# Optimization experiments

Measured on AMD Instinct MI355X. Metric: run time of the kernel, lower is better.

## Reference

```python
import jax, jax.numpy as jnp
import numpy as np

H_FULL, W_FULL = 256, 704
IMG_H, IMG_W = 16, 44  # height//16, width//16
D_BINS, D_STR, D_END = 50, 1.0, 45.0
N_CAMS = 6
BEV_C = 192
VOX_STR = np.array([-40.0, -40.0, -1.0], np.float32)
VOX_END = np.array([40.0, 40.0, 5.4], np.float32)


def _frustum():
    # Faithful to create_pixel_grid: x/y built width-major, flattened, then flat-reshaped
    # to (img_h, img_w) in forward (this scrambling is intentional / matches torch .reshape).
    x = jnp.broadcast_to(jnp.linspace(0.0, W_FULL - 1.0, IMG_W)[:, None], (IMG_W, IMG_H))
    y = jnp.broadcast_to(jnp.linspace(0.0, H_FULL - 1.0, IMG_H)[None, :], (IMG_W, IMG_H))
    pix = jnp.stack([x, y], 0).reshape(2, IMG_H, IMG_W)
    pix = jnp.broadcast_to(pix[:, None], (2, D_BINS, IMG_H, IMG_W))
    d = jnp.broadcast_to(jnp.linspace(D_STR, D_END, D_BINS)[None, :, None, None], (1, D_BINS, IMG_H, IMG_W))
    return jnp.transpose(jnp.concatenate([pix, d], 0), (1, 2, 3, 0))  # [D, h, w, 3]


def trilinear_sample(vol, grid):
    # vol [B,C,D,H,W]; grid [B,Do,Ho,Wo,3] normalized (x,y,z); align_corners=True, zeros padding
    B, C, D, H, W = vol.shape
    Do, Ho, Wo = grid.shape[1:4]
    g = grid.reshape(B, -1, 3)
    P = g.shape[1]
    x = (g[..., 0] + 1.0) * 0.5 * (W - 1)
    y = (g[..., 1] + 1.0) * 0.5 * (H - 1)
    z = (g[..., 2] + 1.0) * 0.5 * (D - 1)
    x0f, y0f, z0f = jnp.floor(x), jnp.floor(y), jnp.floor(z)
    fx, fy, fz = x - x0f, y - y0f, z - z0f
    x0, y0, z0 = x0f.astype(jnp.int32), y0f.astype(jnp.int32), z0f.astype(jnp.int32)
    vol_flat = vol.reshape(B, C, D * H * W)
    gather = jax.vmap(lambda vf, i: jnp.take(vf, i, axis=1))
    out = jnp.zeros((B, C, P), vol.dtype)
    for dz in (0, 1):
        wz = fz if dz else 1.0 - fz
        iz = z0 + dz
        for dy in (0, 1):
            wy = fy if dy else 1.0 - fy
            iy = y0 + dy
            for dx in (0, 1):
                wx = fx if dx else 1.0 - fx
                ix = x0 + dx
                valid = (ix >= 0) & (ix < W) & (iy >= 0) & (iy < H) & (iz >= 0) & (iz < D)
                idx = (jnp.clip(iz, 0, D - 1) * H + jnp.clip(iy, 0, H - 1)) * W + jnp.clip(ix, 0, W - 1)
                v = gather(vol_flat, idx)  # [B,C,P]
                out = out + v * (wx * wy * wz * valid)[:, None, :]
    return out.reshape(B, C, Do, Ho, Wo)


def conv3x3(x, w, b):
    y = jax.lax.conv_general_dilated(x, w, window_strides=(1, 1), padding='SAME',
                                     dimension_numbers=('NCHW', 'OIHW', 'NCHW'))
    return y + b[None, :, None, None]


def setup_inputs() -> dict:
    key = jax.random.key(0)
    ks = jax.random.split(key, 10)
    B = 2
    eye3 = jnp.eye(3, dtype=jnp.float32)
    eye4 = jnp.eye(4, dtype=jnp.float32)
    bev_feat = jax.random.normal(ks[0], (B, BEV_C, 100, 100, 8), jnp.float32)
    imgs = jax.random.normal(ks[1], (B, N_CAMS, 3, H_FULL, W_FULL), jnp.float32)
    sensor2egos = eye4 + 0.1 * jax.random.normal(ks[2], (B, N_CAMS, 4, 4), jnp.float32)
    ego2globals = eye4 + 0.1 * jax.random.normal(ks[3], (B, N_CAMS, 4, 4), jnp.float32)
    K = jnp.array([[700.0, 0.0, 352.0], [0.0, 700.0, 128.0], [0.0, 0.0, 1.0]], jnp.float32)
    intrins = K + 1.0 * jax.random.normal(ks[4], (B, N_CAMS, 3, 3), jnp.float32)
    post_rots = eye3 + 0.01 * jax.random.normal(ks[5], (B, N_CAMS, 3, 3), jnp.float32)
    post_trans = 0.1 * jax.random.normal(ks[6], (B, N_CAMS, 3), jnp.float32)
    bda = eye3 + 0.01 * jax.random.normal(ks[7], (B, 3, 3), jnp.float32)
    enc = BEV_C * D_BINS  # 9600
    conv1_w = 0.003 * jax.random.normal(ks[8], (256, enc, 3, 3), jnp.float32)
    conv1_b = jnp.zeros((256,), jnp.float32)
    conv2_w = 0.02 * jax.random.normal(ks[9], (88, 256, 3, 3), jnp.float32)
    conv2_b = jnp.zeros((88,), jnp.float32)
    return dict(bev_feat=bev_feat, imgs=imgs, sensor2egos=sensor2egos, ego2globals=ego2globals,
                intrins=intrins, post_rots=post_rots, post_trans=post_trans, bda=bda,
                conv1_w=conv1_w, conv1_b=conv1_b, conv2_w=conv2_w, conv2_b=conv2_b)


def reference(bev_feat, imgs, sensor2egos, ego2globals, intrins, post_rots, post_trans, bda,
              conv1_w, conv1_b, conv2_w, conv2_b):
    B = imgs.shape[0]
    vol = jnp.transpose(bev_feat, (0, 1, 4, 3, 2))  # [B,C,Z,Y,X] -> grid_sample (x=W, y=H, z=D)
    fr = _frustum()[None, None]  # [1,1,D,h,w,3]
    pts = fr - post_trans[:, :, None, None, None, :]  # [B,6,D,h,w,3]
    pts = jnp.einsum('bnij,bndhwj->bndhwi', jnp.linalg.inv(post_rots), pts)
    pts = jnp.concatenate([pts[..., :2] * pts[..., 2:3], pts[..., 2:3]], -1)
    pts = jnp.einsum('bnij,bndhwj->bndhwi', jnp.linalg.inv(intrins[:, :N_CAMS]), pts)
    N = D_BINS * IMG_H * IMG_W
    cam = pts.reshape(B, N_CAMS, 3, N)  # faithful flat reshape (same semantics as torch .reshape)
    cam = jnp.concatenate([cam, jnp.ones((B, N_CAMS, 1, N), cam.dtype)], 2)
    ego = jnp.einsum('bnij,bnjp->bnip', sensor2egos[:, :N_CAMS, :3, :], cam)
    ego = jnp.einsum('bij,bnjp->bnip', bda, ego)
    g = jnp.transpose(ego, (0, 1, 3, 2))  # [B,6,N,3]
    vs = jnp.asarray(VOX_STR)
    vl = jnp.asarray(VOX_END - VOX_STR)
    g = (g - vs) / vl * 2.0 - 1.0
    g = g.reshape(B, N_CAMS * D_BINS, IMG_H, IMG_W, 3)  # batch all cams into the depth axis
    s = trilinear_sample(vol, g)  # [B,C,6*D,h,w]
    s = s.reshape(B, BEV_C, N_CAMS, D_BINS, IMG_H, IMG_W)
    s = jnp.transpose(s, (0, 2, 1, 3, 4, 5)).reshape(B * N_CAMS, BEV_C * D_BINS, IMG_H, IMG_W)
    x = jax.nn.relu(conv3x3(s, conv1_w, conv1_b))
    x = jax.nn.relu(conv3x3(x, conv2_w, conv2_b))
    return x  # [B*6, 88, 16, 44] == stack(dim=1).flatten(0,1)
```

## Files before the change

kernel.cpp:

```cpp
#include <hip/hip_runtime.h>
#include <hip/hip_bf16.h>
#include <hip/hip_fp16.h>
#include <stdint.h>

typedef __attribute__((ext_vector_type(8))) short s16x8;
typedef __attribute__((ext_vector_type(4))) float f32x4;
#define BF16 __hip_bfloat16

#define VM0 asm volatile("s_waitcnt vmcnt(0)" ::: "memory")

__device__ __forceinline__ void gload16(void* lds, const void* g) {
  __builtin_amdgcn_global_load_lds((const __attribute__((address_space(1))) void*)g,
                                   (__attribute__((address_space(3))) void*)lds, 16, 0, 0);
}

__device__ __forceinline__ short f2bf(float f) {
  union { __hip_bfloat16 h; short s; } u; u.h = __float2bfloat16(f); return u.s;
}

__device__ __forceinline__ void inv3(const float* m, float* o) {
  float a00=m[0],a01=m[1],a02=m[2],a10=m[3],a11=m[4],a12=m[5],a20=m[6],a21=m[7],a22=m[8];
  float c00 = a11*a22 - a12*a21;
  float c01 = a12*a20 - a10*a22;
  float c02 = a10*a21 - a11*a20;
  float det = a00*c00 + a01*c01 + a02*c02;
  float id = 1.0f/det;
  o[0]=c00*id; o[1]=(a02*a21-a01*a22)*id; o[2]=(a01*a12-a02*a11)*id;
  o[3]=c01*id; o[4]=(a00*a22-a02*a20)*id; o[5]=(a02*a10-a00*a12)*id;
  o[6]=c02*id; o[7]=(a01*a20-a00*a21)*id; o[8]=(a00*a11-a01*a10)*id;
}

__global__ __launch_bounds__(192) void k_prep_vol(const float* __restrict__ bev, BF16* __restrict__ volT) {
  int blk = blockIdx.x;
  int b = blk / 10000, xy = blk % 10000;
  int t = threadIdx.x;
  __shared__ alignas(16) BF16 sm[1536];
  const float* src = bev + (((size_t)b*192 + t)*10000 + xy)*8;
#pragma unroll
  for (int z = 0; z < 8; ++z) sm[z*192 + t] = __float2bfloat16(src[z]);
  __syncthreads();
  BF16* dst = volT + (size_t)blk*1536;
  *reinterpret_cast<s16x8*>(&dst[t*8]) = *reinterpret_cast<const s16x8*>(&sm[t*8]);
}

__global__ __launch_bounds__(256) void k_prep_w1(const float* __restrict__ w1, BF16* __restrict__ A1) {
  int blk = blockIdx.x;
  int oc = blk / 6, c0 = (blk % 6) * 32;
  __shared__ short sm[18000];
  int t = threadIdx.x;
  const float* src = w1 + (size_t)oc*86400 + (size_t)c0*450;
  for (int i = 0; i < 15; ++i) {
    int f4 = i*256 + t;
    if (f4 < 3600) {
      float4 v = *((const float4*)src + f4);
      int flat = f4*4;
#pragma unroll
      for (int q = 0; q < 4; ++q) {
        int fl = flat + q;
        int c = fl / 450, r = fl % 450, dd = r / 9, sg = r % 9;
        float vq = (q==0)?v.x:(q==1)?v.y:(q==2)?v.z:v.w;
        sm[(sg*50 + dd)*40 + c] = f2bf(vq);
      }
    }
  }
  __syncthreads();
  BF16* dstbase = A1 + (size_t)oc*86400 + c0;
  for (int i = 0; i < 8; ++i) {
    int fw = i*256 + t;
    if (fw < 1800) {
      int sdd = fw >> 2, q4 = fw & 3;
      int sg = sdd / 50, dd = sdd % 50;
      s16x8 v = *(const s16x8*)&sm[sdd*40 + q4*8];
      *(s16x8*)&dstbase[(size_t)sg*9600 + dd*192 + q4*8] = v;
    }
  }
}

__global__ __launch_bounds__(256) void k_prep_w2(const float* __restrict__ w2, BF16* __restrict__ w2T) {
  unsigned o = blockIdx.x*256u + threadIdx.x;
  unsigned oc = o / 2304u; unsigned r = o % 2304u;
  unsigned seg = r / 256u; unsigned c = r % 256u;
  float v = (oc < 88u) ? w2[(oc*256u + c)*9u + seg] : 0.0f;
  w2T[o] = __float2bfloat16(v);
}

__global__ __launch_bounds__(256) void k_geom(const float* __restrict__ s2e, const float* __restrict__ intr,
                       const float* __restrict__ prots, const float* __restrict__ ptrans,
                       const float* __restrict__ bda, float* __restrict__ geom) {
  int tid = blockIdx.x*256 + threadIdx.x;
  int p = tid % 35200; int bn = tid / 35200;
  int b = bn / 6;
  float PR[9], IN[9], iPR[9], iIN[9], BD[9], SE[12], PT[3];
#pragma unroll
  for (int i = 0; i < 9; ++i) { PR[i] = prots[bn*9+i]; IN[i] = intr[bn*9+i]; BD[i] = bda[b*9+i]; }
#pragma unroll
  for (int i = 0; i < 12; ++i) SE[i] = s2e[bn*16+i];
#pragma unroll
  for (int i = 0; i < 3; ++i) PT[i] = ptrans[bn*3+i];
  inv3(PR, iPR); inv3(IN, iIN);
  float cam[3];
#pragma unroll
  for (int c3 = 0; c3 < 3; ++c3) {
    int f = c3*35200 + p;
    int comp = f % 3; int t1 = f / 3;
    int w = t1 % 44;  int t2 = t1 / 44;
    int h = t2 % 16;  int dd = t2 / 16;
    int hw = h*44 + w;
    float px = 703.0f*(float)(hw >> 4)*(1.0f/43.0f);
    float py = 17.0f*(float)(hw & 15);
    float dv = 1.0f + 44.0f*(float)dd*(1.0f/49.0f);
    float t0 = px - PT[0], t1f = py - PT[1], t2f = dv - PT[2];
    float ux = iPR[0]*t0 + iPR[1]*t1f + iPR[2]*t2f;
    float uy = iPR[3]*t0 + iPR[4]*t1f + iPR[5]*t2f;
    float uz = iPR[6]*t0 + iPR[7]*t1f + iPR[8]*t2f;
    float m0 = ux*uz, m1 = uy*uz, m2 = uz;
    cam[c3] = iIN[comp*3+0]*m0 + iIN[comp*3+1]*m1 + iIN[comp*3+2]*m2;
  }
  float e0 = SE[0]*cam[0] + SE[1]*cam[1] + SE[2]*cam[2] + SE[3];
  float e1 = SE[4]*cam[0] + SE[5]*cam[1] + SE[6]*cam[2] + SE[7];
  float e2 = SE[8]*cam[0] + SE[9]*cam[1] + SE[10]*cam[2] + SE[11];
  float q0 = BD[0]*e0 + BD[1]*e1 + BD[2]*e2;
  float q1 = BD[3]*e0 + BD[4]*e1 + BD[5]*e2;
  float q2 = BD[6]*e0 + BD[7]*e1 + BD[8]*e2;
  float gx = (q0 + 40.0f)*(1.0f/80.0f)*2.0f - 1.0f;
  float gy = (q1 + 40.0f)*(1.0f/80.0f)*2.0f - 1.0f;
  float gz = (q2 + 1.0f)*(1.0f/6.4f)*2.0f - 1.0f;
  float* o = geom + (size_t)tid*3;
  o[0] = (gx + 1.0f)*0.5f*99.0f;
  o[1] = (gy + 1.0f)*0.5f*99.0f;
  o[2] = (gz + 1.0f)*0.5f*7.0f;
}

__global__ __launch_bounds__(256) void k_sample(const BF16* __restrict__ volT, const float* __restrict__ geom,
                         BF16* __restrict__ s_p) {
  unsigned tid = blockIdx.x*256u + threadIdx.x;
  unsigned cg8 = (tid % 24u) * 8u;
  unsigned q   = tid / 24u;
  unsigned dd  = q % 50u;  unsigned q2 = q / 50u;
  unsigned pix = q2 % 704u; unsigned bn = q2 / 704u;
  unsigned b = bn / 6u;
  const float* g = geom + ((size_t)bn*35200 + dd*704 + pix)*3;
  float X = g[0], Y = g[1], Z = g[2];
  float xf = floorf(X), yf = floorf(Y), zf = floorf(Z);
  int x0 = (int)xf, y0 = (int)yf, z0 = (int)zf;
  float fx = X - xf, fy = Y - yf, fz = Z - zf;
  float acc[8] = {0,0,0,0,0,0,0,0};
#pragma unroll
  for (int dz = 0; dz < 2; ++dz) {
    int iz = z0 + dz; float wz = dz ? fz : 1.0f - fz;
    bool vz = (iz >= 0) && (iz < 8);
    int cz = min(max(iz, 0), 7);
#pragma unroll
    for (int dy = 0; dy < 2; ++dy) {
      int iy = y0 + dy; float wy = dy ? fy : 1.0f - fy;
      bool vy = vz && (iy >= 0) && (iy < 100);
      int cy = min(max(iy, 0), 99);
#pragma unroll
      for (int dx = 0; dx < 2; ++dx) {
        int ix = x0 + dx; float wx = dx ? fx : 1.0f - fx;
        bool vv = vy && (ix >= 0) && (ix < 100);
        int cx = min(max(ix, 0), 99);
        float wgt = wx*wy*wz;
        if (vv && wgt != 0.0f) {
          s16x8 v = *(const s16x8*)&volT[((((size_t)b*100 + cx)*100 + cy)*8 + cz)*192 + cg8];
#pragma unroll
          for (int j = 0; j < 8; ++j) {
            unsigned u = (unsigned)(unsigned short)v[j];
            acc[j] += wgt * __uint_as_float(u << 16);
          }
        }
      }
    }
  }
  s16x8 o;
#pragma unroll
  for (int j = 0; j < 8; ++j) o[j] = f2bf(acc[j]);
  *(s16x8*)&s_p[((size_t)bn*704 + pix)*9600 + dd*192 + cg8] = o;
}

#define G1_NS 180
__global__ __launch_bounds__(256) void k_gemm1(const BF16* __restrict__ A1, const BF16* __restrict__ s_p,
                        const BF16* __restrict__ zpage, __half* __restrict__ part) {
  int gid = blockIdx.x;
  int ks = gid % 15; int t0 = gid / 15;
  int nt = t0 % 6;   t0 /= 6;
  int mt = t0 & 1;   int bn = t0 >> 1;
  int oc0 = mt*128, pix0 = nt*128;
  int tid = threadIdx.x, wv = tid >> 6, lane = tid & 63;
  int wr = wv >> 1, wc = wv & 1;
  __shared__ alignas(16) short lA0s[4096], lA1s[4096], lB0s[4096], lB1s[4096];
  int lr15 = lane & 15, kq8 = (lane >> 4)*8;
  int k0 = ks*5760;
  const BF16* gA0 = A1 + (size_t)(oc0 + wv*32 + lr15)*86400 + k0 + kq8;
  const BF16* gA1 = gA0 + (size_t)16*86400;
  int prow0 = pix0 + wv*32 + lr15;
  int prow1 = prow0 + 16;
  int ph0p = prow0/44, pw0p = prow0%44;
  int ph1p = prow1/44, pw1p = prow1%44;
  int seg  = k0 / 9600;
  int kloc = k0 - seg*9600;
  const BF16 *gB0, *gB1; int inc0, inc1;
  {
    int dh = seg/3 - 1, dw = seg%3 - 1;
    { int qh = ph0p+dh, qw = pw0p+dw;
      bool v = (prow0<704)&&(qh>=0)&&(qh<16)&&(qw>=0)&&(qw<44);
      gB0 = v ? s_p + ((size_t)bn*704 + qh*44+qw)*9600 + kloc + kq8 : zpage + kq8; inc0 = v?32:0; }
    { int qh = ph1p+dh, qw = pw1p+dw;
      bool v = (prow1<704)&&(qh>=0)&&(qh<16)&&(qw>=0)&&(qw<44);
      gB1 = v ? s_p + ((size_t)bn*704 + qh*44+qw)*9600 + kloc + kq8 : zpage + kq8; inc1 = v?32:0; }
  }
#define G1_STAGE(LA, LB) { gload16(&LA[wv*1024], gA0); gload16(&LA[wv*1024+512], gA1); \
                           gload16(&LB[wv*1024], gB0); gload16(&LB[wv*1024+512], gB1); }
#define G1_BUMP() { gA0 += 32; gA1 += 32; gB0 += inc0; gB1 += inc1; kloc += 32; \
    if (kloc == 9600) { kloc = 0; seg++; int sg = seg < 9 ? seg : 8; \
      int dh = sg/3 - 1, dw = sg%3 - 1; \
      { int qh = ph0p+dh, qw = pw0p+dw; bool v = (prow0<704)&&(qh>=0)&&(qh<16)&&(qw>=0)&&(qw<44); \
        gB0 = v ? s_p + ((size_t)bn*704 + qh*44+qw)*9600 + kq8 : zpage + kq8; inc0 = v?32:0; } \
      { int qh = ph1p+dh, qw = pw1p+dw; bool v = (prow1<704)&&(qh>=0)&&(qh<16)&&(qw>=0)&&(qw<44); \
        gB1 = v ? s_p + ((size_t)bn*704 + qh*44+qw)*9600 + kq8 : zpage + kq8; inc1 = v?32:0; } } }
  f32x4 acc[4][4] = {};
  int ra = wr*2048 + lane*8;
  int rb = wc*2048 + lane*8;
#define G1_COMPUTE(LA, LB) { s16x8 af[4], bfv[4]; \
    _Pragma("unroll") for (int m = 0; m < 4; ++m) af[m]  = *(const s16x8*)&LA[ra + m*512]; \
    _Pragma("unroll") for (int n = 0; n < 4; ++n) bfv[n] = *(const s16x8*)&LB[rb + n*512]; \
    _Pragma("unroll") for (int m = 0; m < 4; ++m) \
    _Pragma("unroll") for (int n = 0; n < 4; ++n) \
      acc[m][n] = __builtin_amdgcn_mfma_f32_16x16x32_bf16(af[m], bfv[n], acc[m][n], 0, 0, 0); }

  G1_STAGE(lA0s, lB0s); G1_BUMP();
  VM0;
  __syncthreads();
  for (int t = 0; t < G1_NS; t += 2) {
    G1_STAGE(lA1s, lB1s); G1_BUMP();
    G1_COMPUTE(lA0s, lB0s);
    VM0;
    __syncthreads();
    if (t + 2 < G1_NS) { G1_STAGE(lA0s, lB0s); G1_BUMP(); }
    G1_COMPUTE(lA1s, lB1s);
    VM0;
    __syncthreads();
  }
#pragma unroll
  for (int m = 0; m < 4; ++m) {
    int ocb = oc0 + wr*64 + m*16 + ((lane >> 4) << 2);
#pragma unroll
    for (int n = 0; n < 4; ++n) {
      int px = pix0 + wc*64 + n*16 + lr15;
      if (px < 704) {
        __half* dst = part + (((size_t)ks*12 + bn)*256 + ocb)*704 + px;
#pragma unroll
        for (int r = 0; r < 4; ++r) dst[(size_t)r*704] = __float2half(acc[m][n][r]);
      }
    }
  }
}

__global__ __launch_bounds__(256) void k_reduce1(const __half* __restrict__ part, const float* __restrict__ b1,
                          BF16* __restrict__ out1p) {
  int bn = blockIdx.x / 44; int pg = blockIdx.x % 44; int pix0 = pg*16;
  int t = threadIdx.x;
  __shared__ float sm[4096];
  for (int f = t; f < 4096; f += 256) {
    int oc = f >> 4, pl = f & 15;
    float s = 0.0f;
#pragma unroll
    for (int ks = 0; ks < 15; ++ks)
      s += __half2float(part[(((size_t)ks*12 + bn)*256 + oc)*704 + pix0 + pl]);
    s += b1[oc];
    sm[f] = fmaxf(s, 0.0f);
  }
  __syncthreads();
  for (int f = t; f < 4096; f += 256) {
    int pl = f >> 8;
    int oc = f & 255;
    out1p[((size_t)bn*704 + pix0 + pl)*256 + oc] = __float2bfloat16(sm[oc*16 + pl]);
  }
}

__global__ __launch_bounds__(256) void k_gemm2(const BF16* __restrict__ w2T, const BF16* __restrict__ x1,
                        const BF16* __restrict__ zpage, const float* __restrict__ b2,
                        float* __restrict__ out) {
  int gid = blockIdx.x;
  int nt = gid % 11, bn = gid / 11;
  int pix0 = nt*64;
  int tid = threadIdx.x, wv = tid >> 6, lane = tid & 63;
  int wr = wv >> 1, wc = wv & 1;
  __shared__ alignas(16) short lA[3072];
  __shared__ alignas(16) short lB[2048];
  int lr15 = lane & 15, kq8 = (lane >> 4)*8;
  const BF16* gA0 = w2T + (size_t)(wv*16 + lr15)*2304 + kq8;
  const BF16* gA1 = w2T + (size_t)((4+wv)*16 + lr15)*2304 + kq8;
  int prow = pix0 + wv*16 + lr15;
  int ph0 = prow/44, pw0 = prow%44;
  f32x4 acc[3][2] = {};
  for (int seg = 0; seg < 9; ++seg) {
    int dh = seg/3 - 1, dw = seg%3 - 1;
    int qh = ph0 + dh, qw = pw0 + dw;
    bool v = (qh >= 0) && (qh < 16) && (qw >= 0) && (qw < 44);
    const BF16* gB = v ? x1 + ((size_t)bn*704 + qh*44 + qw)*256 + kq8 : zpage + kq8;
    int incB = v ? 32 : 0;
    for (int s = 0; s < 8; ++s) {
      __syncthreads();
      gload16(&lA[wv*512], gA0);
      if (wv < 2) gload16(&lA[(4+wv)*512], gA1);
      gload16(&lB[wv*512], gB);
      VM0;
      __syncthreads();
      s16x8 af[3], bfv[2];
#pragma unroll
      for (int m = 0; m < 3; ++m) af[m]  = *(const s16x8*)&lA[(wr*3+m)*512 + lane*8];
#pragma unroll
      for (int n = 0; n < 2; ++n) bfv[n] = *(const s16x8*)&lB[(wc*2+n)*512 + lane*8];
#pragma unroll
      for (int m = 0; m < 3; ++m)
#pragma unroll
        for (int n = 0; n < 2; ++n)
          acc[m][n] = __builtin_amdgcn_mfma_f32_16x16x32_bf16(af[m], bfv[n], acc[m][n], 0, 0, 0);
      gA0 += 32; gA1 += 32; gB += incB;
    }
  }
#pragma unroll
  for (int m = 0; m < 3; ++m) {
    int ocb = wr*48 + m*16 + ((lane >> 4) << 2);
#pragma unroll
    for (int n = 0; n < 2; ++n) {
      int px = pix0 + wc*32 + n*16 + lr15;
#pragma unroll
      for (int r = 0; r < 4; ++r) {
        int oc = ocb + r;
        if (oc < 88)
          out[((size_t)bn*88 + oc)*704 + px] = fmaxf(acc[m][n][r] + b2[oc], 0.0f);
      }
    }
  }
}

extern "C" void kernel_launch(void* const* d_in, const int* in_sizes, int n_in,
                              void* d_out, int out_size, void* d_ws, size_t ws_size,
                              hipStream_t stream) {
  (void)in_sizes; (void)n_in; (void)out_size;
  const float* bev   = (const float*)d_in[0];
  const float* s2e   = (const float*)d_in[2];
  const float* intr  = (const float*)d_in[4];
  const float* prots = (const float*)d_in[5];
  const float* ptrns = (const float*)d_in[6];
  const float* bda   = (const float*)d_in[7];
  const float* w1    = (const float*)d_in[8];
  const float* b1    = (const float*)d_in[9];
  const float* w2    = (const float*)d_in[10];
  const float* b2    = (const float*)d_in[11];
  float* out = (float*)d_out;

  char* ws = (char*)d_ws;
  size_t off = 0;
  BF16*   volT  = (BF16*)(ws + off);   off += 61440000;
  BF16*   A1    = (BF16*)(ws + off);   off += 44236800;
  BF16*   w2T   = (BF16*)(ws + off);   off += 442368;
  float*  geom  = (float*)(ws + off);  off += 5068800;
  BF16*   s_p   = (BF16*)(ws + off);   off += 162201600;
  __half* part  = (__half*)(ws + off); off += 64880640;
  BF16*   out1p = (BF16*)(ws + off);   off += 4325376;
  BF16*   zpage = (BF16*)(ws + off);   off += 4096;
  if (off > ws_size) return;

  hipMemsetAsync(zpage, 0, 4096, stream);

  k_prep_vol<<<20000, 192, 0, stream>>>(bev, volT);
  k_prep_w1 <<<1536,  256, 0, stream>>>(w1, A1);
  k_prep_w2 <<<864,   256, 0, stream>>>(w2, w2T);
  k_geom    <<<1650,  256, 0, stream>>>(s2e, intr, prots, ptrns, bda, geom);
  k_sample  <<<39600, 256, 0, stream>>>(volT, geom, s_p);
  k_gemm1   <<<2160,  256, 0, stream>>>(A1, s_p, zpage, part);
  k_reduce1 <<<528,   256, 0, stream>>>(part, b1, out1p);
  k_gemm2   <<<132,   256, 0, stream>>>(w2T, out1p, zpage, b2, out);
}
```

Baseline: 1.334 ms.

## Triple-buffer GEMM1 LDS staging with partial vmcnt waits

Replaces the double-buffered LDS ping-pong in the conv1 implicit GEMM with a three-stage ring. Each compute step now waits only until the oldest stage's loads land (vmcnt(8)) instead of draining all outstanding loads, so two tiles are in flight while one is consumed. This costs 50% more LDS per block, which may lower occupancy, and adds an extra barrier per step.

```diff
diff --git a/kernel.cpp b/kernel.cpp
--- a/kernel.cpp
+++ b/kernel.cpp
@@ -8,6 +8,8 @@
 #define BF16 __hip_bfloat16
 
 #define VM0 asm volatile("s_waitcnt vmcnt(0)" ::: "memory")
+#define VM4 asm volatile("s_waitcnt vmcnt(4)" ::: "memory")
+#define VM8 asm volatile("s_waitcnt vmcnt(8)" ::: "memory")
 
 __device__ __forceinline__ void gload16(void* lds, const void* g) {
   __builtin_amdgcn_global_load_lds((const __attribute__((address_space(1))) void*)g,
@@ -188,7 +190,8 @@
   int oc0 = mt*128, pix0 = nt*128;
   int tid = threadIdx.x, wv = tid >> 6, lane = tid & 63;
   int wr = wv >> 1, wc = wv & 1;
-  __shared__ alignas(16) short lA0s[4096], lA1s[4096], lB0s[4096], lB1s[4096];
+  __shared__ alignas(16) short lsA[3][4096];
+  __shared__ alignas(16) short lsB[3][4096];
   int lr15 = lane & 15, kq8 = (lane >> 4)*8;
   int k0 = ks*5760;
   const BF16* gA0 = A1 + (size_t)(oc0 + wv*32 + lr15)*86400 + k0 + kq8;
@@ -209,8 +212,8 @@
       bool v = (prow1<704)&&(qh>=0)&&(qh<16)&&(qw>=0)&&(qw<44);
       gB1 = v ? s_p + ((size_t)bn*704 + qh*44+qw)*9600 + kloc + kq8 : zpage + kq8; inc1 = v?32:0; }
   }
-#define G1_STAGE(LA, LB) { gload16(&LA[wv*1024], gA0); gload16(&LA[wv*1024+512], gA1); \
-                           gload16(&LB[wv*1024], gB0); gload16(&LB[wv*1024+512], gB1); }
+#define G1_STAGE(i) { gload16(&lsA[i][wv*1024], gA0); gload16(&lsA[i][wv*1024+512], gA1); \
+                      gload16(&lsB[i][wv*1024], gB0); gload16(&lsB[i][wv*1024+512], gB1); }
 #define G1_BUMP() { gA0 += 32; gA1 += 32; gB0 += inc0; gB1 += inc1; kloc += 32; \
     if (kloc == 9600) { kloc = 0; seg++; int sg = seg < 9 ? seg : 8; \
       int dh = sg/3 - 1, dw = sg%3 - 1; \
@@ -221,26 +224,24 @@
   f32x4 acc[4][4] = {};
   int ra = wr*2048 + lane*8;
   int rb = wc*2048 + lane*8;
-#define G1_COMPUTE(LA, LB) { s16x8 af[4], bfv[4]; \
-    _Pragma("unroll") for (int m = 0; m < 4; ++m) af[m]  = *(const s16x8*)&LA[ra + m*512]; \
-    _Pragma("unroll") for (int n = 0; n < 4; ++n) bfv[n] = *(const s16x8*)&LB[rb + n*512]; \
+#define G1_COMPUTE(i) { s16x8 af[4], bfv[4]; \
+    _Pragma("unroll") for (int m = 0; m < 4; ++m) af[m]  = *(const s16x8*)&lsA[i][ra + m*512]; \
+    _Pragma("unroll") for (int n = 0; n < 4; ++n) bfv[n] = *(const s16x8*)&lsB[i][rb + n*512]; \
     _Pragma("unroll") for (int m = 0; m < 4; ++m) \
     _Pragma("unroll") for (int n = 0; n < 4; ++n) \
       acc[m][n] = __builtin_amdgcn_mfma_f32_16x16x32_bf16(af[m], bfv[n], acc[m][n], 0, 0, 0); }
 
-  G1_STAGE(lA0s, lB0s); G1_BUMP();
-  VM0;
-  __syncthreads();
-  for (int t = 0; t < G1_NS; t += 2) {
-    G1_STAGE(lA1s, lB1s); G1_BUMP();
-    G1_COMPUTE(lA0s, lB0s);
-    VM0;
-    __syncthreads();
-    if (t + 2 < G1_NS) { G1_STAGE(lA0s, lB0s); G1_BUMP(); }
-    G1_COMPUTE(lA1s, lB1s);
-    VM0;
-    __syncthreads();
-  }
+  G1_STAGE(0); G1_BUMP();
+  G1_STAGE(1); G1_BUMP();
+  for (int g = 0; g < 59; ++g) {
+    G1_STAGE(2); G1_BUMP(); VM8; __syncthreads(); G1_COMPUTE(0); __syncthreads();
+    G1_STAGE(0); G1_BUMP(); VM8; __syncthreads(); G1_COMPUTE(1); __syncthreads();
+    G1_STAGE(1); G1_BUMP(); VM8; __syncthreads(); G1_COMPUTE(2); __syncthreads();
+  }
+  G1_STAGE(2); VM8; __syncthreads(); G1_COMPUTE(0); __syncthreads();
+  VM4; __syncthreads(); G1_COMPUTE(1); __syncthreads();
+  VM0; __syncthreads(); G1_COMPUTE(2);
+
 #pragma unroll
   for (int m = 0; m < 4; ++m) {
     int ocb = oc0 + wr*64 + m*16 + ((lane >> 4) << 2);
```

Result: no change. 1.311 ms (-1.7%).
